# Kernel optimization log

Measured on AMD Instinct MI355X. Metric: run time of the kernel, lower is better.

The kernel has to match this reference:

```python
import jax, jax.numpy as jnp
import numpy as np

B, N, D = 2, 2048, 256
H, HID, EN = 8, 64, 2
ALPHA = 0.2
NEG = -9e15


def setup_inputs() -> dict:
    key = jax.random.key(0)
    k1, k2, k3, k4, k5, k6 = jax.random.split(key, 6)
    fea_mats = jax.random.normal(k1, (B, N, D), dtype=jnp.float32)
    adj_mats = jax.random.randint(k2, (B, N, N), 0, 2).astype(jnp.float32)
    # xavier-uniform-like init (gain 1.414)
    def xav(k, shape):
        fan_in, fan_out = shape[-2], shape[-1]
        bound = 1.414 * np.sqrt(6.0 / (fan_in + fan_out))
        return jax.random.uniform(k, shape, jnp.float32, -bound, bound)
    W_att = xav(k3, (H, D, HID))          # per-head projection
    a_att = xav(k4, (H, 2 * HID, 1))      # per-head attention vector
    W_last = xav(k5, (H * HID, EN))       # last-layer projection
    a_last = xav(k6, (2 * EN, 1))         # last-layer attention vector
    return {"fea_mats": fea_mats, "adj_mats": adj_mats,
            "W_att": W_att, "a_att": a_att,
            "W_last": W_last, "a_last": a_last}


def _leaky(x):
    return jnp.where(x >= 0, x, ALPHA * x)


def _masked_attn(e, adj):
    # torch: where(adj!=0, e, 0) * adj; masked_fill(==0, -9e15); softmax(dim=1 over columns)
    att = jnp.where(adj != 0, e, jnp.zeros_like(e)) * adj
    att = jnp.where(att == 0, jnp.full_like(att, NEG), att)
    return jax.nn.softmax(att, axis=-1)


def reference(fea_mats, adj_mats, W_att, a_att, W_last, a_last):
    # ---- multi-head GAT layers (concat=True), eval mode -> dropout = identity ----
    wh = jnp.einsum('bnd,hdo->bhno', fea_mats, W_att)        # [B,H,N,HID]
    a1 = a_att[:, :HID, 0]                                   # [H,HID]
    a2 = a_att[:, HID:, 0]                                   # [H,HID]
    e1 = jnp.einsum('bhno,ho->bhn', wh, a1)                  # regulon part
    e2 = jnp.einsum('bhno,ho->bhn', wh, a2)                  # gene part
    e = _leaky(e1[:, :, :, None] + e2[:, :, None, :])        # [B,H,N,N]
    att = _masked_attn(e, adj_mats[:, None])                 # [B,H,N,N]
    x = jax.nn.elu(jnp.einsum('bhnm,bhmo->bhno', att, wh))   # [B,H,N,HID]
    x = jnp.transpose(x, (0, 2, 1, 3)).reshape(B, N, H * HID)
    # ---- last layer (concat=False), adj narrowed to square (already square) ----
    wh2 = jnp.einsum('bnd,de->bne', x, W_last)               # [B,N,EN]
    b1 = a_last[:EN, 0]
    b2 = a_last[EN:, 0]
    e = _leaky(jnp.einsum('bne,e->bn', wh2, b1)[:, :, None]
               + jnp.einsum('bne,e->bn', wh2, b2)[:, None, :])  # [B,N,N]
    att = _masked_attn(e, adj_mats)
    out = jax.nn.elu(jnp.einsum('bnm,bme->bne', att, wh2))   # [B,N,EN]
    return out
```

## Files before the change

### kernel.cpp

```cpp
#include <hip/hip_runtime.h>
#include <hip/hip_bf16.h>
#include <cstdint>
#include <cstddef>

#define B_ 2
#define N_ 2048
#define D_ 256
#define H_ 8
#define HID_ 64
#define EN_ 2
#define ALPHA 0.2f
#define NEGBIG (-3.0e38f)
#define LOG2E 1.4426950408889634f

typedef __bf16 bf16x8 __attribute__((ext_vector_type(8)));
typedef float f32x4 __attribute__((ext_vector_type(4)));
typedef unsigned short ushort8 __attribute__((ext_vector_type(8)));
typedef float float4v __attribute__((ext_vector_type(4)));
typedef float float2v __attribute__((ext_vector_type(2)));

__device__ __forceinline__ unsigned short f2bf(float f) {
    unsigned int u = __builtin_bit_cast(unsigned int, f);
    unsigned int r = u + 0x7FFFu + ((u >> 16) & 1u);
    return (unsigned short)(r >> 16);
}
__device__ __forceinline__ float leakyf(float x) { return fmaxf(x, ALPHA * x); }

__device__ __forceinline__ ushort8 cvt8(const float* __restrict__ p) {
    float4v x0 = *(const float4v*)p;
    float4v x1 = *(const float4v*)(p + 4);
    ushort8 r;
    #pragma unroll
    for (int e = 0; e < 4; ++e) { r[e] = f2bf(x0[e]); r[e + 4] = f2bf(x1[e]); }
    return r;
}

__global__ void k_transpose_w(const float* __restrict__ W,
                              unsigned short* __restrict__ WT) {
    int h = blockIdx.x;
    const float* Wh = W + (size_t)h * D_ * HID_;
    unsigned short* WTh = WT + (size_t)h * HID_ * D_;
    for (int idx = threadIdx.x; idx < D_ * HID_; idx += blockDim.x) {
        int d = idx / HID_, o = idx % HID_;
        WTh[o * D_ + d] = f2bf(Wh[idx]);
    }
}

__global__ __launch_bounds__(256) void k_wh(
    const float* __restrict__ fea,
    const unsigned short* __restrict__ WT,
    const float* __restrict__ a_att,
    unsigned short* __restrict__ whT,
    float* __restrict__ e1, float* __restrict__ e2)
{
    int bid = blockIdx.x;
    int i0 = (bid & 31) << 6;
    int h  = (bid >> 5) & 7;
    int b  = bid >> 8;

    __shared__ __align__(16) union SmemA {
        struct { unsigned short fa[64 * 72]; unsigned short wt[64 * 72]; } s;
        float tr[64 * 65];
    } u;

    int t = threadIdx.x;
    int lane = t & 63;
    int wv = t >> 6;
    int r = lane & 15, q = lane >> 4;
    int ra = t >> 2;
    int cc = (t & 3) * 16;

    f32x4 acc[4] = {};

    const float* fearow = fea + ((size_t)(b * N_ + i0 + ra)) * D_;
    const unsigned short* wtrow = WT + ((size_t)(h * 64 + ra)) * D_;

    for (int d0 = 0; d0 < D_; d0 += 64) {
        *(ushort8*)&u.s.fa[ra * 72 + cc]     = cvt8(fearow + d0 + cc);
        *(ushort8*)&u.s.fa[ra * 72 + cc + 8] = cvt8(fearow + d0 + cc + 8);
        *(ushort8*)&u.s.wt[ra * 72 + cc]     = *(const ushort8*)(wtrow + d0 + cc);
        *(ushort8*)&u.s.wt[ra * 72 + cc + 8] = *(const ushort8*)(wtrow + d0 + cc + 8);
        __syncthreads();
        #pragma unroll
        for (int k0 = 0; k0 < 64; k0 += 32) {
            bf16x8 a = *(const bf16x8*)&u.s.fa[(16 * wv + r) * 72 + k0 + q * 8];
            #pragma unroll
            for (int f = 0; f < 4; ++f) {
                bf16x8 bb = *(const bf16x8*)&u.s.wt[(16 * f + r) * 72 + k0 + q * 8];
                acc[f] = __builtin_amdgcn_mfma_f32_16x16x32_bf16(a, bb, acc[f], 0, 0, 0);
            }
        }
        __syncthreads();
    }

    float a1v[4], a2v[4];
    #pragma unroll
    for (int f = 0; f < 4; ++f) {
        a1v[f] = a_att[h * 128 + 16 * f + r];
        a2v[f] = a_att[h * 128 + 64 + 16 * f + r];
    }
    #pragma unroll
    for (int rr = 0; rr < 4; ++rr) {
        float s1 = 0.f, s2 = 0.f;
        #pragma unroll
        for (int f = 0; f < 4; ++f) { s1 += acc[f][rr] * a1v[f]; s2 += acc[f][rr] * a2v[f]; }
        #pragma unroll
        for (int m = 1; m < 16; m <<= 1) {
            s1 += __shfl_xor(s1, m, 64);
            s2 += __shfl_xor(s2, m, 64);
        }
        if (r == 0) {
            int i = i0 + 16 * wv + 4 * q + rr;
            size_t idx = ((size_t)(b * H_ + h)) * N_ + i;
            e1[idx] = s1 * LOG2E; e2[idx] = s2 * LOG2E;
        }
    }

    #pragma unroll
    for (int f = 0; f < 4; ++f)
        #pragma unroll
        for (int rr = 0; rr < 4; ++rr)
            u.tr[(16 * f + r) * 65 + 16 * wv + 4 * q + rr] = acc[f][rr];
    __syncthreads();
    {
        int o = t >> 2;
        int ch = (t & 3) * 16;
        unsigned short tmp[16];
        #pragma unroll
        for (int e = 0; e < 16; ++e) tmp[e] = f2bf(u.tr[o * 65 + ch + e]);
        ushort8* dst = (ushort8*)(whT + (((size_t)(b * H_ + h) * 64 + o)) * N_ + i0 + ch);
        dst[0] = *(ushort8*)&tmp[0];
        dst[1] = *(ushort8*)&tmp[8];
    }
}

__global__ __launch_bounds__(256) void k_maxe2(const float* __restrict__ e2,
                                               float* __restrict__ mx) {
    int bh = blockIdx.x;
    int t = threadIdx.x;
    const float* row = e2 + (size_t)bh * N_;
    float M = NEGBIG;
    #pragma unroll
    for (int it = 0; it < N_ / 256; ++it) M = fmaxf(M, row[it * 256 + t]);
    #pragma unroll
    for (int s = 1; s < 64; s <<= 1) M = fmaxf(M, __shfl_xor(M, s, 64));
    __shared__ float red[4];
    if ((t & 63) == 0) red[t >> 6] = M;
    __syncthreads();
    if (t == 0) mx[bh] = fmaxf(fmaxf(red[0], red[1]), fmaxf(red[2], red[3]));
}

template<int JPER>
__global__ __launch_bounds__(512, 4) void k_pv1(
    const float* __restrict__ adj,
    const unsigned short* __restrict__ whT,
    const float* __restrict__ e1g, const float* __restrict__ e2g,
    const float* __restrict__ maxE2,
    float* __restrict__ x_part,
    float* __restrict__ zPart)
{
    constexpr int NT = JPER / 64;
    int s  = blockIdx.x;
    int i0 = blockIdx.y << 7;
    int bh = blockIdx.z;
    int h = bh & 7, b = bh >> 3;
    int jBeg = s * JPER;

    __shared__ __align__(16) unsigned short wt_lds[2][64 * 64];
    __shared__ __align__(16) float e2s[2048];

    int t = threadIdx.x;
    int lane = t & 63;
    int wv = t >> 6;
    int r = lane & 15, q = lane >> 4;

    int ir = i0 + 16 * wv + r;
    float eRow = e1g[(size_t)bh * N_ + ir];
    float m = leakyf(eRow + maxE2[bh]);
    float eRm = eRow - m;
    float eR2 = ALPHA * eRow - m;

    const float* e2p = e2g + (size_t)bh * N_ + jBeg;
    const float* ap  = adj + ((size_t)(b * N_ + ir)) * N_ + jBeg + q * 8;
    const unsigned short* wsrc =
        whT + ((size_t)bh * 64 + (t >> 3)) * N_ + jBeg + (t & 7) * 8;
    int woff = (t * 8) ^ (((t >> 3) & 7) << 3);

    int swz = (r & 7) << 3;
    int koff0 = (8 * q) ^ swz;
    int koff1 = (32 + 8 * q) ^ swz;

    bf16x8 ones;
    #pragma unroll
    for (int e = 0; e < 8; ++e) ones[e] = (__bf16)1.0f;

    f32x4 acc[4] = {};
    f32x4 accz = {};

    float4v aA[4], aB[4];
    ushort8 wA, wB;

#define LOADSET(A, W, tile) do {                                           \
        const float* ap_ = ap + (tile) * 64;                               \
        A[0] = *(const float4v*)(ap_);      A[1] = *(const float4v*)(ap_ + 4);  \
        A[2] = *(const float4v*)(ap_ + 32); A[3] = *(const float4v*)(ap_ + 36); \
        W = *(const ushort8*)(wsrc + (tile) * 64);                         \
    } while (0)

    for (int jj = t; jj < JPER; jj += 512) e2s[jj] = e2p[jj];
    LOADSET(aA, wA, 0);
    *(ushort8*)&wt_lds[0][woff] = wA;
    LOADSET(aB, wB, 1);
    __syncthreads();

    auto pgen = [&](const float4v* av, int t8, bf16x8& pa0, bf16x8& pa1) {
        const float* ejs = &e2s[t8 * 64 + q * 8];
        float4v f0 = *(const float4v*)(ejs);
        float4v f1 = *(const float4v*)(ejs + 4);
        float4v g0 = *(const float4v*)(ejs + 32);
        float4v g1 = *(const float4v*)(ejs + 36);
        #pragma unroll
        for (int e = 0; e < 4; ++e) {
            float p;
            p = __builtin_amdgcn_exp2f(fmaxf(eRm + f0[e], __builtin_fmaf(ALPHA, f0[e], eR2)));
            pa0[e] = (__bf16)(p * av[0][e]);
            p = __builtin_amdgcn_exp2f(fmaxf(eRm + f1[e], __builtin_fmaf(ALPHA, f1[e], eR2)));
            pa0[e + 4] = (__bf16)(p * av[1][e]);
            p = __builtin_amdgcn_exp2f(fmaxf(eRm + g0[e], __builtin_fmaf(ALPHA, g0[e], eR2)));
            pa1[e] = (__bf16)(p * av[2][e]);
            p = __builtin_amdgcn_exp2f(fmaxf(eRm + g1[e], __builtin_fmaf(ALPHA, g1[e], eR2)));
            pa1[e + 4] = (__bf16)(p * av[3][e]);
        }
    };

    #pragma unroll 2
    for (int t8 = 0; t8 < NT; ++t8) {
        const int cur = t8 & 1;
        bf16x8 pa0, pa1;
        if (cur == 0) pgen(aA, t8, pa0, pa1);
        else          pgen(aB, t8, pa0, pa1);

        if (t8 + 1 < NT) {
            if (cur == 0) *(ushort8*)&wt_lds[1][woff] = wB;
            else          *(ushort8*)&wt_lds[0][woff] = wA;
        }
        if (t8 + 2 < NT) {
            if (cur == 0) LOADSET(aA, wA, t8 + 2);
            else          LOADSET(aB, wB, t8 + 2);
        }

        const unsigned short* Wb = wt_lds[cur];
        bf16x8 bb;
        #pragma unroll
        for (int f = 0; f < 4; ++f) {
            bb = *(const bf16x8*)&Wb[f * 1024 + r * 64 + koff0];
            acc[f] = __builtin_amdgcn_mfma_f32_16x16x32_bf16(pa0, bb, acc[f], 0, 0, 0);
        }
        accz = __builtin_amdgcn_mfma_f32_16x16x32_bf16(pa0, ones, accz, 0, 0, 0);
        #pragma unroll
        for (int f = 0; f < 4; ++f) {
            bb = *(const bf16x8*)&Wb[f * 1024 + r * 64 + koff1];
            acc[f] = __builtin_amdgcn_mfma_f32_16x16x32_bf16(pa1, bb, acc[f], 0, 0, 0);
        }
        accz = __builtin_amdgcn_mfma_f32_16x16x32_bf16(pa1, ones, accz, 0, 0, 0);
        __syncthreads();
    }
#undef LOADSET

    float* xp = x_part + ((size_t)s * (B_ * N_) + (size_t)b * N_) * 512 + h * 64;
    #pragma unroll
    for (int f = 0; f < 4; ++f) {
        #pragma unroll
        for (int rr = 0; rr < 4; ++rr) {
            int i = i0 + 16 * wv + 4 * q + rr;
            xp[(size_t)i * 512 + 16 * f + r] = acc[f][rr];
        }
    }
    if (r == 0) {
        #pragma unroll
        for (int rr = 0; rr < 4; ++rr) {
            int i = i0 + 16 * wv + 4 * q + rr;
            zPart[((size_t)(s * 16 + bh)) * N_ + i] = accz[rr];
        }
    }
}

__global__ __launch_bounds__(256) void k_wh2(
    const float* __restrict__ x_part,
    const float* __restrict__ zPart,
    const float* __restrict__ W_last,
    const float* __restrict__ a_last,
    float* __restrict__ wh2, float* __restrict__ g1, float* __restrict__ g2,
    int S)
{
    int idx = blockIdx.x * 4 + (threadIdx.x >> 6);
    int lane = threadIdx.x & 63;
    int b = idx >> 11, n = idx & (N_ - 1);
    float a0 = 0.f, a1 = 0.f;
    #pragma unroll
    for (int it = 0; it < 8; ++it) {
        int k = it * 64 + lane;
        float xv = 0.f, zv = 0.f;
        for (int s = 0; s < S; ++s) {
            xv += x_part[((size_t)s * (B_ * N_) + idx) * 512 + k];
            zv += zPart[((size_t)(s * 16 + b * 8 + it)) * N_ + n];
        }
        float x = (zv > 0.f) ? xv / zv : 0.f;
        x = x > 0.f ? x : expm1f(x);
        float2v wl = *(const float2v*)(W_last + k * 2);
        a0 += x * wl[0];
        a1 += x * wl[1];
    }
    #pragma unroll
    for (int s = 1; s < 64; s <<= 1) {
        a0 += __shfl_xor(a0, s, 64);
        a1 += __shfl_xor(a1, s, 64);
    }
    if (lane == 0) {
        wh2[idx * 2] = a0; wh2[idx * 2 + 1] = a1;
        g1[idx] = (a0 * a_last[0] + a1 * a_last[1]) * LOG2E;
        g2[idx] = (a0 * a_last[2] + a1 * a_last[3]) * LOG2E;
    }
}

__global__ __launch_bounds__(256) void k_out(
    const float* __restrict__ adj,
    const float* __restrict__ wh2,
    const float* __restrict__ g1, const float* __restrict__ g2,
    float* __restrict__ out)
{
    int idx = blockIdx.x * 4 + (threadIdx.x >> 6);
    int lane = threadIdx.x & 63;
    int b = idx >> 11;
    float gi = g1[idx];
    const float* arow = adj + (size_t)idx * N_;
    const float* g2b = g2 + (size_t)b * N_;
    const float* wh2b = wh2 + (size_t)b * N_ * 2;

    float ep[32];
    float M = NEGBIG;
    #pragma unroll
    for (int it = 0; it < 8; ++it) {
        int j = it * 256 + lane * 4;
        float4v a4 = *(const float4v*)(arow + j);
        float4v s4 = *(const float4v*)(g2b + j);
        #pragma unroll
        for (int e = 0; e < 4; ++e) {
            float l = leakyf(gi + s4[e]);
            float v = (a4[e] != 0.f) ? l : NEGBIG;
            ep[it * 4 + e] = v;
            M = fmaxf(M, v);
        }
    }
    #pragma unroll
    for (int s = 1; s < 64; s <<= 1) M = fmaxf(M, __shfl_xor(M, s, 64));

    float Z = 0.f, A0 = 0.f, A1 = 0.f;
    #pragma unroll
    for (int it = 0; it < 8; ++it) {
        int j = it * 256 + lane * 4;
        float4v wA = *(const float4v*)(wh2b + 2 * j);
        float4v wB = *(const float4v*)(wh2b + 2 * j + 4);
        #pragma unroll
        for (int e = 0; e < 4; ++e) {
            float p = __builtin_amdgcn_exp2f(ep[it * 4 + e] - M);
            Z += p;
            float w0 = (e < 2) ? wA[2 * e] : wB[2 * (e - 2)];
            float w1 = (e < 2) ? wA[2 * e + 1] : wB[2 * (e - 2) + 1];
            A0 += p * w0;
            A1 += p * w1;
        }
    }
    #pragma unroll
    for (int s = 1; s < 64; s <<= 1) {
        Z += __shfl_xor(Z, s, 64);
        A0 += __shfl_xor(A0, s, 64);
        A1 += __shfl_xor(A1, s, 64);
    }
    if (lane == 0) {
        float o0 = A0 / Z, o1 = A1 / Z;
        o0 = o0 > 0.f ? o0 : expm1f(o0);
        o1 = o1 > 0.f ? o1 : expm1f(o1);
        float2v ov; ov[0] = o0; ov[1] = o1;
        *(float2v*)(out + idx * 2) = ov;
    }
}

extern "C" void kernel_launch(void* const* d_in, const int* in_sizes, int n_in,
                              void* d_out, int out_size, void* d_ws, size_t ws_size,
                              hipStream_t stream) {
    const float* fea    = (const float*)d_in[0];
    const float* adj    = (const float*)d_in[1];
    const float* W_att  = (const float*)d_in[2];
    const float* a_att  = (const float*)d_in[3];
    const float* W_last = (const float*)d_in[4];
    const float* a_last = (const float*)d_in[5];

    char* ws = (char*)d_ws;
    float* e1  = (float*)(ws + 0);
    float* e2  = (float*)(ws + 131072);
    float* mxE = (float*)(ws + 262144);
    float* wh2 = (float*)(ws + 262400);
    float* g1  = (float*)(ws + 295168);
    float* g2  = (float*)(ws + 311552);
    unsigned short* WT  = (unsigned short*)(ws + 327936);
    unsigned short* whT = (unsigned short*)(ws + 590080);
    float* zPart = (float*)(ws + 4784384);
    float* x_part = (float*)(ws + 5308672);

    const size_t BASE = 5308672ULL, XPART = 8388608ULL;
    int S = (ws_size >= BASE + 4 * XPART) ? 4
          : (ws_size >= BASE + 2 * XPART) ? 2 : 1;

    k_transpose_w<<<dim3(H_), dim3(256), 0, stream>>>(W_att, WT);
    k_wh<<<dim3(B_ * H_ * (N_ / 64)), dim3(256), 0, stream>>>(
        fea, WT, a_att, whT, e1, e2);
    k_maxe2<<<dim3(B_ * H_), dim3(256), 0, stream>>>(e2, mxE);
    if (S == 4)
        k_pv1<512><<<dim3(4, N_ / 128, B_ * H_), dim3(512), 0, stream>>>(
            adj, whT, e1, e2, mxE, x_part, zPart);
    else if (S == 2)
        k_pv1<1024><<<dim3(2, N_ / 128, B_ * H_), dim3(512), 0, stream>>>(
            adj, whT, e1, e2, mxE, x_part, zPart);
    else
        k_pv1<2048><<<dim3(1, N_ / 128, B_ * H_), dim3(512), 0, stream>>>(
            adj, whT, e1, e2, mxE, x_part, zPart);
    k_wh2<<<dim3(B_ * N_ / 4), dim3(256), 0, stream>>>(
        x_part, zPart, W_last, a_last, wh2, g1, g2, S);
    k_out<<<dim3(B_ * N_ / 4), dim3(256), 0, stream>>>(
        adj, wh2, g1, g2, (float*)d_out);
}
```

Baseline: 98.78 us.

## Load value tiles directly from global memory and drop LDS staging in attention kernel

The attention-times-value kernel no longer stages the transposed value tile through double-buffered shared memory with per-iteration barriers. Each lane now reads its MFMA B operands straight from global memory, relying on cache for reuse. Blocks shrink from 512 to 256 threads covering 64 rows, doubling the grid. This removes the LDS writes, the swizzle and the per-tile __syncthreads. In exchange each wave issues more global loads with strided access, and value reuse across waves now depends on L1/L2 hits.

```diff
diff --git a/kernel.cpp b/kernel.cpp
--- a/kernel.cpp
+++ b/kernel.cpp
@@ -151,7 +151,7 @@
 }
 
 template<int JPER>
-__global__ __launch_bounds__(512, 4) void k_pv1(
+__global__ __launch_bounds__(256, 4) void k_pv1(
     const float* __restrict__ adj,
     const unsigned short* __restrict__ whT,
     const float* __restrict__ e1g, const float* __restrict__ e2g,
@@ -161,13 +161,12 @@
 {
     constexpr int NT = JPER / 64;
     int s  = blockIdx.x;
-    int i0 = blockIdx.y << 7;
+    int i0 = blockIdx.y << 6;
     int bh = blockIdx.z;
     int h = bh & 7, b = bh >> 3;
     int jBeg = s * JPER;
 
-    __shared__ __align__(16) unsigned short wt_lds[2][64 * 64];
-    __shared__ __align__(16) float e2s[2048];
+    __shared__ float e2s[JPER];
 
     int t = threadIdx.x;
     int lane = t & 63;
@@ -182,13 +181,10 @@
 
     const float* e2p = e2g + (size_t)bh * N_ + jBeg;
     const float* ap  = adj + ((size_t)(b * N_ + ir)) * N_ + jBeg + q * 8;
-    const unsigned short* wsrc =
-        whT + ((size_t)bh * 64 + (t >> 3)) * N_ + jBeg + (t & 7) * 8;
-    int woff = (t * 8) ^ (((t >> 3) & 7) << 3);
-
-    int swz = (r & 7) << 3;
-    int koff0 = (8 * q) ^ swz;
-    int koff1 = (32 + 8 * q) ^ swz;
+    const unsigned short* wp = whT + ((size_t)bh * 64 + r) * N_ + jBeg + q * 8;
+
+    for (int jj = t; jj < JPER; jj += 256) e2s[jj] = e2p[jj];
+    __syncthreads();
 
     bf16x8 ones;
     #pragma unroll
@@ -198,20 +194,15 @@
     f32x4 accz = {};
 
     float4v aA[4], aB[4];
-    ushort8 wA, wB;
-
-#define LOADSET(A, W, tile) do {                                           \
+
+#define LOADADJ(A, tile) do {                                              \
         const float* ap_ = ap + (tile) * 64;                               \
         A[0] = *(const float4v*)(ap_);      A[1] = *(const float4v*)(ap_ + 4);  \
         A[2] = *(const float4v*)(ap_ + 32); A[3] = *(const float4v*)(ap_ + 36); \
-        W = *(const ushort8*)(wsrc + (tile) * 64);                         \
     } while (0)
 
-    for (int jj = t; jj < JPER; jj += 512) e2s[jj] = e2p[jj];
-    LOADSET(aA, wA, 0);
-    *(ushort8*)&wt_lds[0][woff] = wA;
-    LOADSET(aB, wB, 1);
-    __syncthreads();
+    LOADADJ(aA, 0);
+    if (NT > 1) LOADADJ(aB, 1);
 
     auto pgen = [&](const float4v* av, int t8, bf16x8& pa0, bf16x8& pa1) {
         const float* ejs = &e2s[t8 * 64 + q * 8];
@@ -236,36 +227,32 @@
     #pragma unroll 2
     for (int t8 = 0; t8 < NT; ++t8) {
         const int cur = t8 & 1;
+        bf16x8 bb0[4], bb1[4];
+        #pragma unroll
+        for (int f = 0; f < 4; ++f) {
+            bb0[f] = *(const bf16x8*)(wp + (size_t)f * 16 * N_ + t8 * 64);
+            bb1[f] = *(const bf16x8*)(wp + (size_t)f * 16 * N_ + t8 * 64 + 32);
+        }
+
         bf16x8 pa0, pa1;
         if (cur == 0) pgen(aA, t8, pa0, pa1);
         else          pgen(aB, t8, pa0, pa1);
 
-        if (t8 + 1 < NT) {
-            if (cur == 0) *(ushort8*)&wt_lds[1][woff] = wB;
-            else          *(ushort8*)&wt_lds[0][woff] = wA;
-        }
         if (t8 + 2 < NT) {
-            if (cur == 0) LOADSET(aA, wA, t8 + 2);
-            else          LOADSET(aB, wB, t8 + 2);
-        }
-
-        const unsigned short* Wb = wt_lds[cur];
-        bf16x8 bb;
-        #pragma unroll
-        for (int f = 0; f < 4; ++f) {
-            bb = *(const bf16x8*)&Wb[f * 1024 + r * 64 + koff0];
-            acc[f] = __builtin_amdgcn_mfma_f32_16x16x32_bf16(pa0, bb, acc[f], 0, 0, 0);
-        }
+            if (cur == 0) LOADADJ(aA, t8 + 2);
+            else          LOADADJ(aB, t8 + 2);
+        }
+
+        #pragma unroll
+        for (int f = 0; f < 4; ++f)
+            acc[f] = __builtin_amdgcn_mfma_f32_16x16x32_bf16(pa0, bb0[f], acc[f], 0, 0, 0);
         accz = __builtin_amdgcn_mfma_f32_16x16x32_bf16(pa0, ones, accz, 0, 0, 0);
         #pragma unroll
-        for (int f = 0; f < 4; ++f) {
-            bb = *(const bf16x8*)&Wb[f * 1024 + r * 64 + koff1];
-            acc[f] = __builtin_amdgcn_mfma_f32_16x16x32_bf16(pa1, bb, acc[f], 0, 0, 0);
-        }
+        for (int f = 0; f < 4; ++f)
+            acc[f] = __builtin_amdgcn_mfma_f32_16x16x32_bf16(pa1, bb1[f], acc[f], 0, 0, 0);
         accz = __builtin_amdgcn_mfma_f32_16x16x32_bf16(pa1, ones, accz, 0, 0, 0);
-        __syncthreads();
-    }
-#undef LOADSET
+    }
+#undef LOADADJ
 
     float* xp = x_part + ((size_t)s * (B_ * N_) + (size_t)b * N_) * 512 + h * 64;
     #pragma unroll
@@ -417,13 +404,13 @@
         fea, WT, a_att, whT, e1, e2);
     k_maxe2<<<dim3(B_ * H_), dim3(256), 0, stream>>>(e2, mxE);
     if (S == 4)
-        k_pv1<512><<<dim3(4, N_ / 128, B_ * H_), dim3(512), 0, stream>>>(
+        k_pv1<512><<<dim3(4, N_ / 64, B_ * H_), dim3(256), 0, stream>>>(
             adj, whT, e1, e2, mxE, x_part, zPart);
     else if (S == 2)
-        k_pv1<1024><<<dim3(2, N_ / 128, B_ * H_), dim3(512), 0, stream>>>(
+        k_pv1<1024><<<dim3(2, N_ / 64, B_ * H_), dim3(256), 0, stream>>>(
             adj, whT, e1, e2, mxE, x_part, zPart);
     else
-        k_pv1<2048><<<dim3(1, N_ / 128, B_ * H_), dim3(512), 0, stream>>>(
+        k_pv1<2048><<<dim3(1, N_ / 64, B_ * H_), dim3(256), 0, stream>>>(
             adj, whT, e1, e2, mxE, x_part, zPart);
     k_wh2<<<dim3(B_ * N_ / 4), dim3(256), 0, stream>>>(
         x_part, zPart, W_last, a_last, wh2, g1, g2, S);
```

After: 162.4 us. 1.64x slower.
